# Performance work log

Hardware: AMD Instinct MI355X
Metric: run time of the kernel (lower is better)

Reference implementation:

```python
import jax, jax.numpy as jnp
import numpy as np

N = 100000   # nodes
E = 800000   # edges
IN = 128     # input feature dim
H = 2        # heads
C = 64       # hidden_dim (per-head channels)
OUT = 40     # classes
L = 3        # num_layers
EPS = 1e-16  # matches torch_geometric.utils.softmax denominator eps


def setup_inputs() -> dict:
    key = jax.random.key(0)
    ks = jax.random.split(key, 4 * L + 6)
    inp = {}
    inp["x"] = jax.random.normal(ks[0], (N, IN), dtype=jnp.float32)
    inp["edge_index"] = jax.random.randint(ks[1], (2, E), 0, N, dtype=jnp.int32)
    dims = [IN] + [H * C] * (L - 1)
    ki = 2
    for l in range(L):
        d = dims[l]
        inp[f"W{l}"] = jax.random.normal(ks[ki], (H * C, d), dtype=jnp.float32) / np.float32(np.sqrt(d)); ki += 1
        inp[f"b{l}"] = jnp.zeros((H * C,), dtype=jnp.float32)
        inp[f"al{l}"] = jax.random.normal(ks[ki], (H, C), dtype=jnp.float32) * 0.1; ki += 1
        inp[f"ar{l}"] = jax.random.normal(ks[ki], (H, C), dtype=jnp.float32) * 0.1; ki += 1
    inp["Wp1"] = jax.random.normal(ks[ki], (C, H * C), dtype=jnp.float32) / np.float32(np.sqrt(H * C)); ki += 1
    inp["bp1"] = jnp.zeros((C,), dtype=jnp.float32)
    inp["Wp2"] = jax.random.normal(ks[ki], (OUT, C), dtype=jnp.float32) / np.float32(np.sqrt(C)); ki += 1
    inp["bp2"] = jnp.zeros((OUT,), dtype=jnp.float32)
    return inp


def _gat_layer(x, W, b, al, ar, src, dst):
    # lin_l == lin_r (shared weights in the original)
    h = (x @ W.T + b).reshape(-1, H, C)          # [N, H, C]
    alpha_l = al * h                              # source-side scores [N, H, C]
    alpha_r = ar * h                              # target-side scores [N, H, C]
    # per-edge raw attention logits; NOTE: original computes leaky_relu(alpha)
    # but then applies softmax to the RAW sum (faithful to source code).
    e = alpha_r[dst] + alpha_l[src]               # [E, H, C]
    m = jax.ops.segment_max(e, dst, num_segments=N)
    w = jnp.exp(e - m[dst])
    s = jax.ops.segment_sum(w, dst, num_segments=N)
    att = w / (s[dst] + EPS)                      # segment softmax per target node
    out = jax.ops.segment_sum(att * h[src], dst, num_segments=N)  # [N, H, C]
    return out.reshape(-1, H * C)


def reference(x, edge_index, W0, b0, al0, ar0, W1, b1, al1, ar1, W2, b2, al2, ar2,
              Wp1, bp1, Wp2, bp2):
    src, dst = edge_index[0], edge_index[1]
    layers = [(W0, b0, al0, ar0), (W1, b1, al1, ar1), (W2, b2, al2, ar2)]
    h = x
    for (W, b, al, ar) in layers:
        h = _gat_layer(h, W, b, al, ar, src, dst)
        h = jax.nn.relu(h)  # dropout p=0 -> identity
    h = h @ Wp1.T + bp1
    h = h @ Wp2.T + bp2
    return jax.nn.log_softmax(h, axis=1)
```

## Files before the change

kernel.cpp:

```cpp
#include <hip/hip_runtime.h>
#include <hip/hip_bf16.h>
#include <math.h>

#define NN 100000
#define EE 800000
#define DD 128
#define OUTC 40

constexpr int NBUCK = (NN + 511) >> 9;
constexpr int BCAP  = 6144;
constexpr int EB    = 2048;

typedef short bf16x8 __attribute__((ext_vector_type(8)));
typedef float f32x4 __attribute__((ext_vector_type(4)));

__device__ __forceinline__ ushort f2bf(float f) {
  unsigned u = __float_as_uint(f);
  u = (u + 0x7FFFu + ((u >> 16) & 1u)) >> 16;
  return (ushort)u;
}
__device__ __forceinline__ float bflo(unsigned u) { return __uint_as_float(u << 16); }
__device__ __forceinline__ float bfhi(unsigned u) { return __uint_as_float(u & 0xFFFF0000u); }

__device__ __forceinline__ int swz(int row, int kbyte) {
  return row * 256 + (kbyte ^ ((row & 7) << 4));
}
__device__ __forceinline__ int swz128(int row, int kbyte) {
  return row * 128 + (kbyte ^ ((row & 7) << 4));
}

__global__ __launch_bounds__(256) void k_initcur(int* __restrict__ cursor0) {
  int b = threadIdx.x;
  if (b < NBUCK) cursor0[b] = b * BCAP;
}

__global__ __launch_bounds__(256) void k_binA(const int* __restrict__ src, const int* __restrict__ dst,
                                              int* __restrict__ cursor0, int2* __restrict__ binned, int e) {
  __shared__ int cnt[NBUCK], base[NBUCK], cnt2[NBUCK];
  int t = threadIdx.x;
  for (int b = t; b < NBUCK; b += 256) { cnt[b] = 0; cnt2[b] = 0; }
  __syncthreads();
  int e0 = blockIdx.x * EB;
#pragma unroll
  for (int p = 0; p < EB / 256; ++p) {
    int i = e0 + p * 256 + t;
    if (i < e) atomicAdd(&cnt[dst[i] >> 9], 1);
  }
  __syncthreads();
  for (int b = t; b < NBUCK; b += 256)
    if (cnt[b] > 0) base[b] = atomicAdd(&cursor0[b], cnt[b]);
  __syncthreads();
#pragma unroll
  for (int p = 0; p < EB / 256; ++p) {
    int i = e0 + p * 256 + t;
    if (i < e) {
      int d = dst[i];
      int bk = d >> 9;
      int pos = base[bk] + atomicAdd(&cnt2[bk], 1);
      binned[pos] = make_int2(src[i], d);
    }
  }
}

__global__ __launch_bounds__(256) void k_degB(const int* __restrict__ cursor0,
                                              const int2* __restrict__ binned,
                                              int* __restrict__ deg, int n) {
  __shared__ int cnt[512];
  int b = blockIdx.x, t = threadIdx.x;
  cnt[t] = 0; cnt[t + 256] = 0;
  __syncthreads();
  int node0 = b << 9;
  int beg = b * BCAP;
  int cend = cursor0[b];
  for (int i = beg + t; i < cend; i += 256)
    atomicAdd(&cnt[binned[i].y - node0], 1);
  __syncthreads();
  if (node0 + t < n) deg[node0 + t] = cnt[t];
  if (node0 + t + 256 < n) deg[node0 + t + 256] = cnt[t + 256];
}

__global__ __launch_bounds__(1024) void k_scan1(const int* __restrict__ deg, int* __restrict__ rp,
                                                int* __restrict__ bsum, int n) {
  __shared__ int s[1024];
  int t = threadIdx.x;
  int i = blockIdx.x * 1024 + t;
  s[t] = (i < n) ? deg[i] : 0;
  __syncthreads();
  for (int off = 1; off < 1024; off <<= 1) {
    int x = (t >= off) ? s[t - off] : 0;
    __syncthreads();
    s[t] += x;
    __syncthreads();
  }
  if (i < n) rp[i + 1] = s[t];
  if (t == 1023) bsum[blockIdx.x] = s[1023];
}

__global__ __launch_bounds__(128) void k_scan2(int* __restrict__ bsum, int nb) {
  __shared__ int s[128];
  int t = threadIdx.x;
  s[t] = (t < nb) ? bsum[t] : 0;
  __syncthreads();
  for (int off = 1; off < 128; off <<= 1) {
    int x = (t >= off) ? s[t - off] : 0;
    __syncthreads();
    s[t] += x;
    __syncthreads();
  }
  if (t < nb) bsum[t] = s[t];
}

__global__ void k_scan3(int* __restrict__ rp, const int* __restrict__ bsum, int n) {
  int i = blockIdx.x * 256 + threadIdx.x;
  if (i == 0) rp[0] = 0;
  if (i < n) {
    int blk = i >> 10;
    rp[i + 1] = rp[i + 1] + ((blk > 0) ? bsum[blk - 1] : 0);
  }
}

__global__ __launch_bounds__(256) void k_scatC(const int* __restrict__ cursor0,
                                               const int2* __restrict__ binned,
                                               const int* __restrict__ rp,
                                               int* __restrict__ col, int n) {
  __shared__ int cur[512];
  __shared__ int lrp[512];
  int b = blockIdx.x, t = threadIdx.x;
  cur[t] = 0; cur[t + 256] = 0;
  int node0 = b << 9;
  lrp[t] = (node0 + t < n) ? rp[node0 + t] : 0;
  lrp[t + 256] = (node0 + t + 256 < n) ? rp[node0 + t + 256] : 0;
  __syncthreads();
  int beg = b * BCAP;
  int cend = cursor0[b];
  for (int i = beg + t; i < cend; i += 256) {
    int2 p = binned[i];
    int d = p.y - node0;
    int pos = lrp[d] + atomicAdd(&cur[d], 1);
    col[pos] = p.x;
  }
}

template<bool INF32>
__global__ __launch_bounds__(256, 2) void k_mfma_gemm(const void* __restrict__ xin,
                                                      const float* __restrict__ W,
                                                      const float* __restrict__ bias,
                                                      ushort* __restrict__ outp, int n) {
  __shared__ __align__(16) char lds[65536];
  const int t = threadIdx.x;
  const int node0 = blockIdx.x * 128;

  if (INF32) {
#pragma unroll
    for (int p = 0; p < 16; ++p) {
      int F = p * 256 + t;
      int r = F >> 5, cchunk = F & 31;
      int node = node0 + r;
      float4 v = make_float4(0.f, 0.f, 0.f, 0.f);
      if (node < n) v = *(const float4*)((const float*)xin + (size_t)node * DD + cchunk * 4);
      ushort q[4] = {f2bf(v.x), f2bf(v.y), f2bf(v.z), f2bf(v.w)};
      *(unsigned long long*)(lds + swz(r, cchunk * 8)) = *(unsigned long long*)q;
    }
  } else {
#pragma unroll
    for (int p = 0; p < 8; ++p) {
      int F = p * 256 + t;
      int r = F >> 4, cchunk = F & 15;
      int node = node0 + r;
      uint4 v = make_uint4(0u, 0u, 0u, 0u);
      if (node < n) v = *(const uint4*)((const ushort*)xin + (size_t)node * DD + cchunk * 8);
      *(uint4*)(lds + swz(r, cchunk * 16)) = v;
    }
  }
  {
#pragma unroll
    for (int p = 0; p < 16; ++p) {
      int F = p * 256 + t;
      int r = F >> 5, cchunk = F & 31;
      float4 v = *(const float4*)(W + (size_t)r * DD + cchunk * 4);
      ushort q[4] = {f2bf(v.x), f2bf(v.y), f2bf(v.z), f2bf(v.w)};
      *(unsigned long long*)(lds + 32768 + swz(r, cchunk * 8)) = *(unsigned long long*)q;
    }
  }
  __syncthreads();

  const int lane = t & 63;
  const int l15 = lane & 15;
  const int lkb = (lane >> 4) * 16;
  const int wrow0 = (t >> 6) * 32;

  f32x4 acc[2][8];
#pragma unroll
  for (int j = 0; j < 8; ++j) {
    float bv = bias[j * 16 + l15];
    acc[0][j] = (f32x4){bv, bv, bv, bv};
    acc[1][j] = (f32x4){bv, bv, bv, bv};
  }

#pragma unroll
  for (int c = 0; c < 4; ++c) {
    bf16x8 a0 = *(const bf16x8*)(lds + swz(wrow0 + l15, c * 64 + lkb));
    bf16x8 a1 = *(const bf16x8*)(lds + swz(wrow0 + 16 + l15, c * 64 + lkb));
#pragma unroll
    for (int j = 0; j < 8; ++j) {
      bf16x8 b = *(const bf16x8*)(lds + 32768 + swz(j * 16 + l15, c * 64 + lkb));
      acc[0][j] = __builtin_amdgcn_mfma_f32_16x16x32_bf16(a0, b, acc[0][j], 0, 0, 0);
      acc[1][j] = __builtin_amdgcn_mfma_f32_16x16x32_bf16(a1, b, acc[1][j], 0, 0, 0);
    }
  }

  const int rbase = wrow0 + (lane >> 4) * 4;
#pragma unroll
  for (int i = 0; i < 2; ++i) {
#pragma unroll
    for (int r = 0; r < 4; ++r) {
      int node = node0 + rbase + i * 16 + r;
      if (node < n) {
#pragma unroll
        for (int j = 0; j < 8; ++j)
          outp[(size_t)node * DD + j * 16 + l15] = f2bf(acc[i][j][r]);
      }
    }
  }
}

__global__ __launch_bounds__(256) void k_gat_agg(const ushort* __restrict__ h, const int* __restrict__ rp,
                                                 const int* __restrict__ col, const float* __restrict__ al,
                                                 const float* __restrict__ ar, ushort* __restrict__ out, int n) {
  int node = blockIdx.x * 4 + (threadIdx.x >> 6);
  int lane = threadIdx.x & 63;
  if (node >= n) return;
  const unsigned* hu = (const unsigned*)h;
  float al0 = al[2 * lane], al1 = al[2 * lane + 1];
  unsigned ud = hu[(unsigned)(node * 64 + lane)];
  float base0 = ar[2 * lane] * bflo(ud);
  float base1 = ar[2 * lane + 1] * bfhi(ud);
  int beg = __builtin_amdgcn_readfirstlane(rp[node]);
  int end = __builtin_amdgcn_readfirstlane(rp[node + 1]);
  float num0 = 0.f, num1 = 0.f, den0 = 0.f, den1 = 0.f;
#define ACCUM(U) { \
    float h0 = bflo(U), h1 = bfhi(U); \
    float w0 = __expf(fmaf(al0, h0, base0)); \
    float w1 = __expf(fmaf(al1, h1, base1)); \
    den0 += w0; den1 += w1; \
    num0 = fmaf(w0, h0, num0); num1 = fmaf(w1, h1, num1); }
  int j = beg;
  for (; j + 8 <= end; j += 8) {
    int s0 = __builtin_amdgcn_readfirstlane(col[j]);
    int s1 = __builtin_amdgcn_readfirstlane(col[j + 1]);
    int s2 = __builtin_amdgcn_readfirstlane(col[j + 2]);
    int s3 = __builtin_amdgcn_readfirstlane(col[j + 3]);
    int s4 = __builtin_amdgcn_readfirstlane(col[j + 4]);
    int s5 = __builtin_amdgcn_readfirstlane(col[j + 5]);
    int s6 = __builtin_amdgcn_readfirstlane(col[j + 6]);
    int s7 = __builtin_amdgcn_readfirstlane(col[j + 7]);
    unsigned u0 = hu[(unsigned)(s0 * 64 + lane)];
    unsigned u1 = hu[(unsigned)(s1 * 64 + lane)];
    unsigned u2 = hu[(unsigned)(s2 * 64 + lane)];
    unsigned u3 = hu[(unsigned)(s3 * 64 + lane)];
    unsigned u4 = hu[(unsigned)(s4 * 64 + lane)];
    unsigned u5 = hu[(unsigned)(s5 * 64 + lane)];
    unsigned u6 = hu[(unsigned)(s6 * 64 + lane)];
    unsigned u7 = hu[(unsigned)(s7 * 64 + lane)];
    ACCUM(u0); ACCUM(u1); ACCUM(u2); ACCUM(u3);
    ACCUM(u4); ACCUM(u5); ACCUM(u6); ACCUM(u7);
  }
  for (; j + 4 <= end; j += 4) {
    int s0 = __builtin_amdgcn_readfirstlane(col[j]);
    int s1 = __builtin_amdgcn_readfirstlane(col[j + 1]);
    int s2 = __builtin_amdgcn_readfirstlane(col[j + 2]);
    int s3 = __builtin_amdgcn_readfirstlane(col[j + 3]);
    unsigned u0 = hu[(unsigned)(s0 * 64 + lane)];
    unsigned u1 = hu[(unsigned)(s1 * 64 + lane)];
    unsigned u2 = hu[(unsigned)(s2 * 64 + lane)];
    unsigned u3 = hu[(unsigned)(s3 * 64 + lane)];
    ACCUM(u0); ACCUM(u1); ACCUM(u2); ACCUM(u3);
  }
  for (; j + 2 <= end; j += 2) {
    int s0 = __builtin_amdgcn_readfirstlane(col[j]);
    int s1 = __builtin_amdgcn_readfirstlane(col[j + 1]);
    unsigned u0 = hu[(unsigned)(s0 * 64 + lane)];
    unsigned u1 = hu[(unsigned)(s1 * 64 + lane)];
    ACCUM(u0); ACCUM(u1);
  }
  for (; j < end; ++j) {
    int s = __builtin_amdgcn_readfirstlane(col[j]);
    unsigned u = hu[(unsigned)(s * 64 + lane)];
    ACCUM(u);
  }
#undef ACCUM
  float o0 = fmaxf(num0 / (den0 + 1e-16f), 0.f);
  float o1 = fmaxf(num1 / (den1 + 1e-16f), 0.f);
  ((unsigned*)out)[(unsigned)(node * 64 + lane)] = (unsigned)f2bf(o0) | ((unsigned)f2bf(o1) << 16);
}

__global__ __launch_bounds__(256, 2) void k_final_fused(const ushort* __restrict__ xin,
                                                        const float* __restrict__ W1,
                                                        const float* __restrict__ b1,
                                                        const float* __restrict__ Wp2,
                                                        const float* __restrict__ bp2,
                                                        float* __restrict__ out, int n) {
  __shared__ __align__(16) char lds[49152];
  const int t = threadIdx.x;
  const int node0 = blockIdx.x * 128;
  const int lane = t & 63;
  const int l15 = lane & 15;
  const int lg = lane >> 4;
  const int lkb = lg * 16;
  const int wrow0 = (t >> 6) * 32;

#pragma unroll
  for (int p = 0; p < 8; ++p) {
    int F = p * 256 + t;
    int r = F >> 4, cchunk = F & 15;
    int node = node0 + r;
    uint4 v = make_uint4(0u, 0u, 0u, 0u);
    if (node < n) v = *(const uint4*)(xin + (size_t)node * DD + cchunk * 8);
    *(uint4*)(lds + swz(r, cchunk * 16)) = v;
  }
#pragma unroll
  for (int p = 0; p < 8; ++p) {
    int F = p * 256 + t;
    int r = F >> 5, cchunk = F & 31;
    float4 v = *(const float4*)(W1 + (size_t)r * DD + cchunk * 4);
    ushort q[4] = {f2bf(v.x), f2bf(v.y), f2bf(v.z), f2bf(v.w)};
    *(unsigned long long*)(lds + 32768 + swz(r, cchunk * 8)) = *(unsigned long long*)q;
  }
  __syncthreads();

  f32x4 acc[2][4];
#pragma unroll
  for (int j = 0; j < 4; ++j) {
    float bv = b1[j * 16 + l15];
    acc[0][j] = (f32x4){bv, bv, bv, bv};
    acc[1][j] = (f32x4){bv, bv, bv, bv};
  }
#pragma unroll
  for (int c = 0; c < 4; ++c) {
    bf16x8 a0 = *(const bf16x8*)(lds + swz(wrow0 + l15, c * 64 + lkb));
    bf16x8 a1 = *(const bf16x8*)(lds + swz(wrow0 + 16 + l15, c * 64 + lkb));
#pragma unroll
    for (int j = 0; j < 4; ++j) {
      bf16x8 b = *(const bf16x8*)(lds + 32768 + swz(j * 16 + l15, c * 64 + lkb));
      acc[0][j] = __builtin_amdgcn_mfma_f32_16x16x32_bf16(a0, b, acc[0][j], 0, 0, 0);
      acc[1][j] = __builtin_amdgcn_mfma_f32_16x16x32_bf16(a1, b, acc[1][j], 0, 0, 0);
    }
  }
  __syncthreads();

  char* h1L = lds;
  char* wpL = lds + 16384;
  const int rbase = wrow0 + lg * 4;
#pragma unroll
  for (int i = 0; i < 2; ++i)
#pragma unroll
    for (int r = 0; r < 4; ++r) {
      int row = rbase + i * 16 + r;
#pragma unroll
      for (int j = 0; j < 4; ++j)
        *(ushort*)(h1L + swz128(row, (j * 16 + l15) * 2)) = f2bf(acc[i][j][r]);
    }
#pragma unroll
  for (int p = 0; p < 3; ++p) {
    int flat = p * 1024 + t * 4;
    int row = flat >> 6, ch0 = flat & 63;
    float4 v = make_float4(0.f, 0.f, 0.f, 0.f);
    if (row < OUTC) v = *(const float4*)(Wp2 + row * 64 + ch0);
    ushort q[4] = {f2bf(v.x), f2bf(v.y), f2bf(v.z), f2bf(v.w)};
    *(unsigned long long*)(wpL + swz128(row, ch0 * 2)) = *(unsigned long long*)q;
  }
  __syncthreads();

  f32x4 acc2[2][3];
#pragma unroll
  for (int j = 0; j < 3; ++j) {
    int cls = j * 16 + l15;
    float bv = (cls < OUTC) ? bp2[cls] : -1e30f;
    acc2[0][j] = (f32x4){bv, bv, bv, bv};
    acc2[1][j] = (f32x4){bv, bv, bv, bv};
  }
#pragma unroll
  for (int c2 = 0; c2 < 2; ++c2) {
    bf16x8 a0 = *(const bf16x8*)(h1L + swz128(wrow0 + l15, c2 * 64 + lkb));
    bf16x8 a1 = *(const bf16x8*)(h1L + swz128(wrow0 + 16 + l15, c2 * 64 + lkb));
#pragma unroll
    for (int j = 0; j < 3; ++j) {
      bf16x8 b = *(const bf16x8*)(wpL + swz128(j * 16 + l15, c2 * 64 + lkb));
      acc2[0][j] = __builtin_amdgcn_mfma_f32_16x16x32_bf16(a0, b, acc2[0][j], 0, 0, 0);
      acc2[1][j] = __builtin_amdgcn_mfma_f32_16x16x32_bf16(a1, b, acc2[1][j], 0, 0, 0);
    }
  }

#pragma unroll
  for (int i = 0; i < 2; ++i) {
#pragma unroll
    for (int r = 0; r < 4; ++r) {
      float u0 = acc2[i][0][r], u1 = acc2[i][1][r], u2 = acc2[i][2][r];
      float m = fmaxf(fmaxf(u0, u1), u2);
#pragma unroll
      for (int d = 1; d < 16; d <<= 1) m = fmaxf(m, __shfl_xor(m, d, 64));
      float s = __expf(u0 - m) + __expf(u1 - m) + __expf(u2 - m);
#pragma unroll
      for (int d = 1; d < 16; d <<= 1) s += __shfl_xor(s, d, 64);
      float ls = __logf(s) + m;
      int node = node0 + rbase + i * 16 + r;
      if (node < n) {
        float* op = out + (size_t)node * OUTC;
        op[l15] = u0 - ls;
        op[16 + l15] = u1 - ls;
        if (l15 < 8) op[32 + l15] = u2 - ls;
      }
    }
  }
}

extern "C" void kernel_launch(void* const* d_in, const int* in_sizes, int n_in,
                              void* d_out, int out_size, void* d_ws, size_t ws_size,
                              hipStream_t stream) {
  const float* x   = (const float*)d_in[0];
  const int*   ei  = (const int*)d_in[1];
  const float* W[3]  = {(const float*)d_in[2],  (const float*)d_in[6],  (const float*)d_in[10]};
  const float* B[3]  = {(const float*)d_in[3],  (const float*)d_in[7],  (const float*)d_in[11]};
  const float* AL[3] = {(const float*)d_in[4],  (const float*)d_in[8],  (const float*)d_in[12]};
  const float* AR[3] = {(const float*)d_in[5],  (const float*)d_in[9],  (const float*)d_in[13]};
  const float* Wp1 = (const float*)d_in[14];
  const float* bp1 = (const float*)d_in[15];
  const float* Wp2 = (const float*)d_in[16];
  const float* bp2 = (const float*)d_in[17];
  float* outp = (float*)d_out;

  const int n = NN, e = EE;
  const int* srcp = ei;
  const int* dstp = ei + e;

  char* ws = (char*)d_ws;
  size_t off = 0;
  auto alloc = [&](size_t bytes) { void* p = ws + off; off = (off + bytes + 255) & ~(size_t)255; return p; };
  ushort* bhA = (ushort*)alloc((size_t)n * DD * 2);
  ushort* bhB = (ushort*)alloc((size_t)n * DD * 2);
  int*   deg   = (int*)alloc((size_t)n * 4);
  int*   rp    = (int*)alloc((size_t)(n + 1) * 4);
  int*   bsum  = (int*)alloc(1024 * 4);
  int*   col   = (int*)alloc((size_t)e * 4);
  int*   cursor0 = (int*)alloc((size_t)NBUCK * 4);
  int2*  binned  = (int2*)alloc((size_t)NBUCK * BCAP * 8);
  (void)ws_size;

  k_initcur<<<1, 256, 0, stream>>>(cursor0);
  k_binA<<<(e + EB - 1) / EB, 256, 0, stream>>>(srcp, dstp, cursor0, binned, e);
  k_degB<<<NBUCK, 256, 0, stream>>>(cursor0, binned, deg, n);
  int nb = (n + 1023) / 1024;
  k_scan1<<<nb, 1024, 0, stream>>>(deg, rp, bsum, n);
  k_scan2<<<1, 128, 0, stream>>>(bsum, nb);
  k_scan3<<<(n + 255) / 256, 256, 0, stream>>>(rp, bsum, n);
  k_scatC<<<NBUCK, 256, 0, stream>>>(cursor0, binned, rp, col, n);

  const int gblocks = (n + 127) / 128;
  const int ablocks = (n + 3) / 4;
  k_mfma_gemm<true><<<gblocks, 256, 0, stream>>>(x, W[0], B[0], bhA, n);
  k_gat_agg<<<ablocks, 256, 0, stream>>>(bhA, rp, col, AL[0], AR[0], bhB, n);
  for (int l = 1; l < 3; ++l) {
    k_mfma_gemm<false><<<gblocks, 256, 0, stream>>>(bhB, W[l], B[l], bhA, n);
    k_gat_agg<<<ablocks, 256, 0, stream>>>(bhA, rp, col, AL[l], AR[l], bhB, n);
  }
  k_final_fused<<<gblocks, 256, 0, stream>>>(bhB, Wp1, bp1, Wp2, bp2, outp, n);
}
```

Before: 345.6 us.

## Fuse CSR build into bucket-local scan and load edge indices per wavefront

Replaces the degree, three-pass scan and scatter kernels with a single-block bucket-offset scan plus one per-bucket kernel. That kernel histograms destinations, scans them locally, writes row pointers and scatters columns, cutting five launches and a pass over the binned edges down to two. The aggregation kernel now loads up to 64 column indices with one vector load and broadcasts them via readlane, instead of scalar loads per edge. It also folds log2(e) into the attention coefficients so it can use exp2f. The CSR column order within a node may differ, which changes floating-point summation order slightly.

```diff
diff --git a/kernel.cpp b/kernel.cpp
--- a/kernel.cpp
+++ b/kernel.cpp
@@ -62,81 +62,55 @@
   }
 }
 
-__global__ __launch_bounds__(256) void k_degB(const int* __restrict__ cursor0,
-                                              const int2* __restrict__ binned,
-                                              int* __restrict__ deg, int n) {
-  __shared__ int cnt[512];
-  int b = blockIdx.x, t = threadIdx.x;
-  cnt[t] = 0; cnt[t + 256] = 0;
-  __syncthreads();
-  int node0 = b << 9;
-  int beg = b * BCAP;
-  int cend = cursor0[b];
-  for (int i = beg + t; i < cend; i += 256)
-    atomicAdd(&cnt[binned[i].y - node0], 1);
-  __syncthreads();
-  if (node0 + t < n) deg[node0 + t] = cnt[t];
-  if (node0 + t + 256 < n) deg[node0 + t + 256] = cnt[t + 256];
-}
-
-__global__ __launch_bounds__(1024) void k_scan1(const int* __restrict__ deg, int* __restrict__ rp,
-                                                int* __restrict__ bsum, int n) {
-  __shared__ int s[1024];
+__global__ __launch_bounds__(256) void k_bbase(const int* __restrict__ cursor0, int* __restrict__ bbase) {
+  __shared__ int s[256];
   int t = threadIdx.x;
-  int i = blockIdx.x * 1024 + t;
-  s[t] = (i < n) ? deg[i] : 0;
-  __syncthreads();
-  for (int off = 1; off < 1024; off <<= 1) {
+  int c = (t < NBUCK) ? (cursor0[t] - t * BCAP) : 0;
+  s[t] = c;
+  __syncthreads();
+  for (int off = 1; off < 256; off <<= 1) {
     int x = (t >= off) ? s[t - off] : 0;
     __syncthreads();
     s[t] += x;
     __syncthreads();
   }
-  if (i < n) rp[i + 1] = s[t];
-  if (t == 1023) bsum[blockIdx.x] = s[1023];
-}
-
-__global__ __launch_bounds__(128) void k_scan2(int* __restrict__ bsum, int nb) {
-  __shared__ int s[128];
-  int t = threadIdx.x;
-  s[t] = (t < nb) ? bsum[t] : 0;
-  __syncthreads();
-  for (int off = 1; off < 128; off <<= 1) {
-    int x = (t >= off) ? s[t - off] : 0;
+  if (t < NBUCK) bbase[t] = s[t] - c;
+}
+
+__global__ __launch_bounds__(256) void k_bucket(const int* __restrict__ cursor0,
+                                                const int* __restrict__ bbase,
+                                                const int2* __restrict__ binned,
+                                                int* __restrict__ rp, int* __restrict__ col, int n) {
+  __shared__ int hist[512], scn[512], cur[512];
+  int b = blockIdx.x, t = threadIdx.x;
+  hist[t] = 0; hist[t + 256] = 0;
+  __syncthreads();
+  int node0 = b << 9;
+  int beg = b * BCAP, cend = cursor0[b];
+  for (int i = beg + t; i < cend; i += 256)
+    atomicAdd(&hist[binned[i].y - node0], 1);
+  __syncthreads();
+  scn[t] = hist[t]; scn[t + 256] = hist[t + 256];
+  __syncthreads();
+  for (int off = 1; off < 512; off <<= 1) {
+    int a0 = (t >= off) ? scn[t - off] : 0;
+    int a1 = scn[t + 256 - off];
     __syncthreads();
-    s[t] += x;
+    scn[t] += a0;
+    scn[t + 256] += a1;
     __syncthreads();
   }
-  if (t < nb) bsum[t] = s[t];
-}
-
-__global__ void k_scan3(int* __restrict__ rp, const int* __restrict__ bsum, int n) {
-  int i = blockIdx.x * 256 + threadIdx.x;
-  if (i == 0) rp[0] = 0;
-  if (i < n) {
-    int blk = i >> 10;
-    rp[i + 1] = rp[i + 1] + ((blk > 0) ? bsum[blk - 1] : 0);
-  }
-}
-
-__global__ __launch_bounds__(256) void k_scatC(const int* __restrict__ cursor0,
-                                               const int2* __restrict__ binned,
-                                               const int* __restrict__ rp,
-                                               int* __restrict__ col, int n) {
-  __shared__ int cur[512];
-  __shared__ int lrp[512];
-  int b = blockIdx.x, t = threadIdx.x;
-  cur[t] = 0; cur[t + 256] = 0;
-  int node0 = b << 9;
-  lrp[t] = (node0 + t < n) ? rp[node0 + t] : 0;
-  lrp[t + 256] = (node0 + t + 256 < n) ? rp[node0 + t + 256] : 0;
-  __syncthreads();
-  int beg = b * BCAP;
-  int cend = cursor0[b];
+  int base = bbase[b];
+  int e0 = scn[t] - hist[t];
+  int e1 = scn[t + 256] - hist[t + 256];
+  cur[t] = e0; cur[t + 256] = e1;
+  if (node0 + t <= n) rp[node0 + t] = base + e0;
+  if (node0 + t + 256 <= n) rp[node0 + t + 256] = base + e1;
+  __syncthreads();
   for (int i = beg + t; i < cend; i += 256) {
     int2 p = binned[i];
     int d = p.y - node0;
-    int pos = lrp[d] + atomicAdd(&cur[d], 1);
+    int pos = base + atomicAdd(&cur[d], 1);
     col[pos] = p.x;
   }
 }
@@ -231,62 +205,69 @@
   int lane = threadIdx.x & 63;
   if (node >= n) return;
   const unsigned* hu = (const unsigned*)h;
-  float al0 = al[2 * lane], al1 = al[2 * lane + 1];
+  const float L2E = 1.44269504f;
+  float al0 = al[2 * lane] * L2E, al1 = al[2 * lane + 1] * L2E;
   unsigned ud = hu[(unsigned)(node * 64 + lane)];
-  float base0 = ar[2 * lane] * bflo(ud);
-  float base1 = ar[2 * lane + 1] * bfhi(ud);
+  float base0 = ar[2 * lane] * L2E * bflo(ud);
+  float base1 = ar[2 * lane + 1] * L2E * bfhi(ud);
   int beg = __builtin_amdgcn_readfirstlane(rp[node]);
   int end = __builtin_amdgcn_readfirstlane(rp[node + 1]);
+  int deg = end - beg;
   float num0 = 0.f, num1 = 0.f, den0 = 0.f, den1 = 0.f;
 #define ACCUM(U) { \
     float h0 = bflo(U), h1 = bfhi(U); \
-    float w0 = __expf(fmaf(al0, h0, base0)); \
-    float w1 = __expf(fmaf(al1, h1, base1)); \
+    float w0 = exp2f(fmaf(al0, h0, base0)); \
+    float w1 = exp2f(fmaf(al1, h1, base1)); \
     den0 += w0; den1 += w1; \
     num0 = fmaf(w0, h0, num0); num1 = fmaf(w1, h1, num1); }
-  int j = beg;
-  for (; j + 8 <= end; j += 8) {
-    int s0 = __builtin_amdgcn_readfirstlane(col[j]);
-    int s1 = __builtin_amdgcn_readfirstlane(col[j + 1]);
-    int s2 = __builtin_amdgcn_readfirstlane(col[j + 2]);
-    int s3 = __builtin_amdgcn_readfirstlane(col[j + 3]);
-    int s4 = __builtin_amdgcn_readfirstlane(col[j + 4]);
-    int s5 = __builtin_amdgcn_readfirstlane(col[j + 5]);
-    int s6 = __builtin_amdgcn_readfirstlane(col[j + 6]);
-    int s7 = __builtin_amdgcn_readfirstlane(col[j + 7]);
-    unsigned u0 = hu[(unsigned)(s0 * 64 + lane)];
-    unsigned u1 = hu[(unsigned)(s1 * 64 + lane)];
-    unsigned u2 = hu[(unsigned)(s2 * 64 + lane)];
-    unsigned u3 = hu[(unsigned)(s3 * 64 + lane)];
-    unsigned u4 = hu[(unsigned)(s4 * 64 + lane)];
-    unsigned u5 = hu[(unsigned)(s5 * 64 + lane)];
-    unsigned u6 = hu[(unsigned)(s6 * 64 + lane)];
-    unsigned u7 = hu[(unsigned)(s7 * 64 + lane)];
-    ACCUM(u0); ACCUM(u1); ACCUM(u2); ACCUM(u3);
-    ACCUM(u4); ACCUM(u5); ACCUM(u6); ACCUM(u7);
-  }
-  for (; j + 4 <= end; j += 4) {
-    int s0 = __builtin_amdgcn_readfirstlane(col[j]);
-    int s1 = __builtin_amdgcn_readfirstlane(col[j + 1]);
-    int s2 = __builtin_amdgcn_readfirstlane(col[j + 2]);
-    int s3 = __builtin_amdgcn_readfirstlane(col[j + 3]);
-    unsigned u0 = hu[(unsigned)(s0 * 64 + lane)];
-    unsigned u1 = hu[(unsigned)(s1 * 64 + lane)];
-    unsigned u2 = hu[(unsigned)(s2 * 64 + lane)];
-    unsigned u3 = hu[(unsigned)(s3 * 64 + lane)];
-    ACCUM(u0); ACCUM(u1); ACCUM(u2); ACCUM(u3);
-  }
-  for (; j + 2 <= end; j += 2) {
-    int s0 = __builtin_amdgcn_readfirstlane(col[j]);
-    int s1 = __builtin_amdgcn_readfirstlane(col[j + 1]);
-    unsigned u0 = hu[(unsigned)(s0 * 64 + lane)];
-    unsigned u1 = hu[(unsigned)(s1 * 64 + lane)];
-    ACCUM(u0); ACCUM(u1);
-  }
-  for (; j < end; ++j) {
-    int s = __builtin_amdgcn_readfirstlane(col[j]);
-    unsigned u = hu[(unsigned)(s * 64 + lane)];
-    ACCUM(u);
+  for (int c0 = 0; c0 < deg; c0 += 64) {
+    int m = deg - c0; if (m > 64) m = 64;
+    int idx = c0 + lane; if (idx >= deg) idx = deg - 1;
+    int vcol = col[beg + idx];
+    int j = 0;
+    for (; j + 8 <= m; j += 8) {
+      int s0 = __builtin_amdgcn_readlane(vcol, j + 0);
+      int s1 = __builtin_amdgcn_readlane(vcol, j + 1);
+      int s2 = __builtin_amdgcn_readlane(vcol, j + 2);
+      int s3 = __builtin_amdgcn_readlane(vcol, j + 3);
+      int s4 = __builtin_amdgcn_readlane(vcol, j + 4);
+      int s5 = __builtin_amdgcn_readlane(vcol, j + 5);
+      int s6 = __builtin_amdgcn_readlane(vcol, j + 6);
+      int s7 = __builtin_amdgcn_readlane(vcol, j + 7);
+      unsigned u0 = hu[(unsigned)(s0 * 64 + lane)];
+      unsigned u1 = hu[(unsigned)(s1 * 64 + lane)];
+      unsigned u2 = hu[(unsigned)(s2 * 64 + lane)];
+      unsigned u3 = hu[(unsigned)(s3 * 64 + lane)];
+      unsigned u4 = hu[(unsigned)(s4 * 64 + lane)];
+      unsigned u5 = hu[(unsigned)(s5 * 64 + lane)];
+      unsigned u6 = hu[(unsigned)(s6 * 64 + lane)];
+      unsigned u7 = hu[(unsigned)(s7 * 64 + lane)];
+      ACCUM(u0); ACCUM(u1); ACCUM(u2); ACCUM(u3);
+      ACCUM(u4); ACCUM(u5); ACCUM(u6); ACCUM(u7);
+    }
+    for (; j + 4 <= m; j += 4) {
+      int s0 = __builtin_amdgcn_readlane(vcol, j + 0);
+      int s1 = __builtin_amdgcn_readlane(vcol, j + 1);
+      int s2 = __builtin_amdgcn_readlane(vcol, j + 2);
+      int s3 = __builtin_amdgcn_readlane(vcol, j + 3);
+      unsigned u0 = hu[(unsigned)(s0 * 64 + lane)];
+      unsigned u1 = hu[(unsigned)(s1 * 64 + lane)];
+      unsigned u2 = hu[(unsigned)(s2 * 64 + lane)];
+      unsigned u3 = hu[(unsigned)(s3 * 64 + lane)];
+      ACCUM(u0); ACCUM(u1); ACCUM(u2); ACCUM(u3);
+    }
+    for (; j + 2 <= m; j += 2) {
+      int s0 = __builtin_amdgcn_readlane(vcol, j + 0);
+      int s1 = __builtin_amdgcn_readlane(vcol, j + 1);
+      unsigned u0 = hu[(unsigned)(s0 * 64 + lane)];
+      unsigned u1 = hu[(unsigned)(s1 * 64 + lane)];
+      ACCUM(u0); ACCUM(u1);
+    }
+    for (; j < m; ++j) {
+      int s0 = __builtin_amdgcn_readlane(vcol, j);
+      unsigned u0 = hu[(unsigned)(s0 * 64 + lane)];
+      ACCUM(u0);
+    }
   }
 #undef ACCUM
   float o0 = fmaxf(num0 / (den0 + 1e-16f), 0.f);
@@ -438,22 +419,17 @@
   auto alloc = [&](size_t bytes) { void* p = ws + off; off = (off + bytes + 255) & ~(size_t)255; return p; };
   ushort* bhA = (ushort*)alloc((size_t)n * DD * 2);
   ushort* bhB = (ushort*)alloc((size_t)n * DD * 2);
-  int*   deg   = (int*)alloc((size_t)n * 4);
   int*   rp    = (int*)alloc((size_t)(n + 1) * 4);
-  int*   bsum  = (int*)alloc(1024 * 4);
   int*   col   = (int*)alloc((size_t)e * 4);
   int*   cursor0 = (int*)alloc((size_t)NBUCK * 4);
+  int*   bbase   = (int*)alloc((size_t)NBUCK * 4);
   int2*  binned  = (int2*)alloc((size_t)NBUCK * BCAP * 8);
   (void)ws_size;
 
   k_initcur<<<1, 256, 0, stream>>>(cursor0);
   k_binA<<<(e + EB - 1) / EB, 256, 0, stream>>>(srcp, dstp, cursor0, binned, e);
-  k_degB<<<NBUCK, 256, 0, stream>>>(cursor0, binned, deg, n);
-  int nb = (n + 1023) / 1024;
-  k_scan1<<<nb, 1024, 0, stream>>>(deg, rp, bsum, n);
-  k_scan2<<<1, 128, 0, stream>>>(bsum, nb);
-  k_scan3<<<(n + 255) / 256, 256, 0, stream>>>(rp, bsum, n);
-  k_scatC<<<NBUCK, 256, 0, stream>>>(cursor0, binned, rp, col, n);
+  k_bbase<<<1, 256, 0, stream>>>(cursor0, bbase);
+  k_bucket<<<NBUCK, 256, 0, stream>>>(cursor0, bbase, binned, rp, col, n);
 
   const int gblocks = (n + 127) / 128;
   const int ablocks = (n + 3) / 4;
```

Measured after the change: 367.3 us. +6.3%, slower.
